# Optimization experiments

Measured on AMD Instinct MI355X. Metric: run time of the kernel, lower is better.

The kernel has to match this reference:

```python
import jax, jax.numpy as jnp
import numpy as np

DIM = 96
HEADS = 6
HEAD_DIM = DIM // HEADS
WIN = 8
N = WIN * WIN           # tokens per window
B_ = 4096               # num_windows * batch
TABLE = (2 * WIN - 1) ** 2  # 225


def setup_inputs() -> dict:
    key = jax.random.key(0)
    ks = jax.random.split(key, 7)
    x = jax.random.normal(ks[0], (B_, N, DIM), dtype=jnp.float32)
    rpi = jax.random.randint(ks[1], (N, N), 0, TABLE)
    qkv_w = jax.random.normal(ks[2], (3 * DIM, DIM), dtype=jnp.float32) * 0.02
    qkv_b = jnp.zeros((3 * DIM,), dtype=jnp.float32)
    proj_w = jax.random.normal(ks[3], (DIM, DIM), dtype=jnp.float32) * 0.02
    proj_b = jnp.zeros((DIM,), dtype=jnp.float32)
    rpb_table = jax.random.normal(ks[4], (TABLE, HEADS), dtype=jnp.float32) * 0.02
    return {"x": x, "rpi": rpi, "qkv_w": qkv_w, "qkv_b": qkv_b,
            "proj_w": proj_w, "proj_b": proj_b, "rpb_table": rpb_table}


def reference(x, rpi, qkv_w, qkv_b, proj_w, proj_b, rpb_table):
    b_, n, c = x.shape
    scale = HEAD_DIM ** -0.5
    # qkv projection: (b_, n, 3, H, hd)
    qkv = (x @ qkv_w.T + qkv_b).reshape(b_, n, 3, HEADS, HEAD_DIM)
    qkv = jnp.transpose(qkv, (2, 0, 3, 1, 4))  # (3, b_, H, n, hd)
    q, k, v = qkv[0], qkv[1], qkv[2]
    attn = jnp.einsum('bhnd,bhmd->bhnm', q * scale, k)
    # relative position bias gather: (n, n, H) -> (H, n, n)
    bias = jnp.transpose(rpb_table[rpi], (2, 0, 1))
    attn = jax.nn.softmax(attn + bias[None], axis=-1)
    out = jnp.einsum('bhnm,bhmd->bnhd', attn, v).reshape(b_, n, c)
    return out @ proj_w.T + proj_b
```

## Files before the change

kernel.cpp:

```cpp
#include <hip/hip_runtime.h>

#define NWIN 4096
#define DIM 96
#define HEADS 6
#define NTOK 64

typedef __bf16 bf16x8 __attribute__((ext_vector_type(8)));
typedef __bf16 bf16x4 __attribute__((ext_vector_type(4)));
typedef short  s16x4  __attribute__((ext_vector_type(4)));
typedef float  f32x4  __attribute__((ext_vector_type(4)));

#define WS_QKVW 0
#define WS_PROJW 55296
#define WS_BIAS 73728
#define WS_TOTAL 172032

__device__ __forceinline__ f32x4 mfma32(bf16x8 a, bf16x8 b, f32x4 c) {
  return __builtin_amdgcn_mfma_f32_16x16x32_bf16(a, b, c, 0, 0, 0);
}
__device__ __forceinline__ f32x4 mfma16k(bf16x4 a, bf16x4 b, f32x4 c) {
  return __builtin_amdgcn_mfma_f32_16x16x16bf16_1k(
      __builtin_bit_cast(s16x4, a), __builtin_bit_cast(s16x4, b), c, 0, 0, 0);
}

__device__ __forceinline__ bf16x8 cvt8(const float* p) {
  const float4* q = (const float4*)p;
  float4 a = q[0];
  float4 b = q[1];
  bf16x8 r;
  r[0] = (__bf16)a.x; r[1] = (__bf16)a.y; r[2] = (__bf16)a.z; r[3] = (__bf16)a.w;
  r[4] = (__bf16)b.x; r[5] = (__bf16)b.y; r[6] = (__bf16)b.z; r[7] = (__bf16)b.w;
  return r;
}

__global__ void prep_kernel(const float* __restrict__ qkv_w,
                            const float* __restrict__ proj_w,
                            const float* __restrict__ rpb,
                            const int* __restrict__ rpi,
                            char* __restrict__ ws) {
  int i = blockIdx.x * blockDim.x + threadIdx.x;
  __bf16* qw = (__bf16*)(ws + WS_QKVW);
  __bf16* pw = (__bf16*)(ws + WS_PROJW);
  float* bias = (float*)(ws + WS_BIAS);
  if (i < 288 * 96) qw[i] = (__bf16)qkv_w[i];
  int j = i - 288 * 96;
  if (j >= 0 && j < 96 * 96) pw[j] = (__bf16)proj_w[j];
  int t = i - (288 * 96 + 96 * 96);
  if (t >= 0 && t < HEADS * 16 * 64 * 4) {
    int r = t & 3;
    int lane = (t >> 2) & 63;
    int ba = (t >> 8) & 15;
    int h = t >> 12;
    int bq = ba >> 2, a = ba & 3;
    int l16 = lane & 15, lq = lane >> 4;
    int qrow = 16 * bq + l16;
    int kcol = 16 * a + 4 * lq + r;
    bias[t] = rpb[rpi[qrow * 64 + kcol] * HEADS + h];
  }
}

template <bool USE_WS>
__global__ __launch_bounds__(768, 4) void win_attn(
    const float* __restrict__ x,
    const int* __restrict__ rpi,
    const float* __restrict__ qkv_w,
    const float* __restrict__ qkv_b,
    const float* __restrict__ proj_w,
    const float* __restrict__ proj_b,
    const float* __restrict__ rpb,
    const char* __restrict__ ws,
    float* __restrict__ out) {
  __shared__ __align__(16) __bf16 lds[2 * 6656];

  const int tid = (int)threadIdx.x;
  const int wv = tid >> 6;
  const int win = wv / 6;
  const int h = wv - 6 * win;
  const int lane = tid & 63;
  const int l16 = lane & 15;
  const int lq = lane >> 4;
  const int b = 2 * (int)blockIdx.x + win;

  __bf16* xfrag = lds + win * 6656;
  __bf16* ao = xfrag;

  const float* xw = x + (size_t)b * (NTOK * DIM);
  const __bf16* qwb = (const __bf16*)(ws + WS_QKVW);
  const __bf16* pwb = (const __bf16*)(ws + WS_PROJW);
  const float4* bias4 = (const float4*)(ws + WS_BIAS) + (h << 10);

#pragma unroll
  for (int ff = 0; ff < 2; ++ff) {
    const int f = 2 * h + ff;
    const int mt = f / 3, ks = f - 3 * mt;
    bf16x8 v = cvt8(xw + (16 * mt + l16) * DIM + 32 * ks + 8 * lq);
    *(bf16x8*)(xfrag + (f * 64 + lane) * 8) = v;
  }
  __syncthreads();

#define XV(mt, ks) (*(const bf16x8*)(xfrag + (((mt) * 3 + (ks)) * 64 + lane) * 8))

  bf16x4 kb[4];
  {
    const int frow = (HEADS + h) * 16;
    bf16x8 wb[3];
#pragma unroll
    for (int ks = 0; ks < 3; ++ks) {
      if constexpr (USE_WS)
        wb[ks] = *(const bf16x8*)(qwb + (frow + l16) * 96 + 32 * ks + 8 * lq);
      else
        wb[ks] = cvt8(qkv_w + (frow + l16) * 96 + 32 * ks + 8 * lq);
    }
    const float4 kb4 = *(const float4*)(qkv_b + frow + 4 * lq);
    const float kbv[4] = {kb4.x, kb4.y, kb4.z, kb4.w};
#pragma unroll
    for (int mt = 0; mt < 4; ++mt) {
      f32x4 acc = {0.f, 0.f, 0.f, 0.f};
#pragma unroll
      for (int ks = 0; ks < 3; ++ks) acc = mfma32(wb[ks], XV(mt, ks), acc);
#pragma unroll
      for (int r = 0; r < 4; ++r) kb[mt][r] = (__bf16)(acc[r] + kbv[r]);
    }
  }

  bf16x4 qv4[4];
  {
    const int frow = h * 16;
    bf16x8 wb[3];
#pragma unroll
    for (int ks = 0; ks < 3; ++ks) {
      if constexpr (USE_WS)
        wb[ks] = *(const bf16x8*)(qwb + (frow + l16) * 96 + 32 * ks + 8 * lq);
      else
        wb[ks] = cvt8(qkv_w + (frow + l16) * 96 + 32 * ks + 8 * lq);
    }
    const float4 qb4 = *(const float4*)(qkv_b + frow + 4 * lq);
    const float qbv[4] = {qb4.x, qb4.y, qb4.z, qb4.w};
#pragma unroll
    for (int mt = 0; mt < 4; ++mt) {
      f32x4 acc = {0.f, 0.f, 0.f, 0.f};
#pragma unroll
      for (int ks = 0; ks < 3; ++ks) acc = mfma32(wb[ks], XV(mt, ks), acc);
#pragma unroll
      for (int r = 0; r < 4; ++r) qv4[mt][r] = (__bf16)((acc[r] + qbv[r]) * 0.25f);
    }
  }

  bf16x4 vb4[4];
  {
    const int frow = (2 * HEADS + h) * 16;
    bf16x8 wb[3];
#pragma unroll
    for (int ks = 0; ks < 3; ++ks) {
      if constexpr (USE_WS)
        wb[ks] = *(const bf16x8*)(qwb + (frow + l16) * 96 + 32 * ks + 8 * lq);
      else
        wb[ks] = cvt8(qkv_w + (frow + l16) * 96 + 32 * ks + 8 * lq);
    }
    const float vb = qkv_b[frow + l16];
#pragma unroll
    for (int mt = 0; mt < 4; ++mt) {
      f32x4 acc = {0.f, 0.f, 0.f, 0.f};
#pragma unroll
      for (int ks = 0; ks < 3; ++ks) acc = mfma32(XV(mt, ks), wb[ks], acc);
#pragma unroll
      for (int r = 0; r < 4; ++r) vb4[mt][r] = (__bf16)(acc[r] + vb);
    }
  }
#undef XV
  __syncthreads();

#pragma unroll
  for (int bq = 0; bq < 4; ++bq) {
    f32x4 s[4];
    if constexpr (USE_WS) {
#pragma unroll
      for (int a = 0; a < 4; ++a) {
        float4 t = bias4[(bq * 4 + a) * 64 + lane];
        s[a][0] = t.x; s[a][1] = t.y; s[a][2] = t.z; s[a][3] = t.w;
      }
    } else {
#pragma unroll
      for (int a = 0; a < 4; ++a)
#pragma unroll
        for (int r = 0; r < 4; ++r)
          s[a][r] = rpb[rpi[(16 * bq + l16) * 64 + 16 * a + 4 * lq + r] * HEADS + h];
    }

#pragma unroll
    for (int a = 0; a < 4; ++a) s[a] = mfma16k(kb[a], qv4[bq], s[a]);

    float tp[4];
    bf16x4 pa[4];
#pragma unroll
    for (int a = 0; a < 4; ++a) {
      float t0 = 0.f;
#pragma unroll
      for (int r = 0; r < 4; ++r) {
        const __bf16 pe = (__bf16)__expf(s[a][r]);
        pa[a][r] = pe;
        t0 += (float)pe;
      }
      tp[a] = t0;
    }
    float tsum = (tp[0] + tp[1]) + (tp[2] + tp[3]);
    tsum += __shfl_xor(tsum, 16);
    tsum += __shfl_xor(tsum, 32);

    f32x4 oacc = {0.f, 0.f, 0.f, 0.f};
#pragma unroll
    for (int a = 0; a < 4; ++a) oacc = mfma16k(pa[a], vb4[a], oacc);

    const float rv = 1.0f / tsum;
#pragma unroll
    for (int r = 0; r < 4; ++r)
      ao[(16 * bq + 4 * lq + r) * 104 + 16 * h + l16] = (__bf16)(oacc[r] * rv);
  }
  __syncthreads();

  bf16x8 wpb[3];
#pragma unroll
  for (int ks = 0; ks < 3; ++ks) {
    if constexpr (USE_WS)
      wpb[ks] = *(const bf16x8*)(pwb + (16 * h + l16) * 96 + 32 * ks + 8 * lq);
    else
      wpb[ks] = cvt8(proj_w + (16 * h + l16) * 96 + 32 * ks + 8 * lq);
  }
  const float pb2 = proj_b[16 * h + l16];
  float* outw = out + (size_t)b * (NTOK * DIM);
#pragma unroll
  for (int mt = 0; mt < 4; ++mt) {
    f32x4 acc = {0.f, 0.f, 0.f, 0.f};
#pragma unroll
    for (int ks = 0; ks < 3; ++ks) {
      bf16x8 aa = *(const bf16x8*)(ao + (16 * mt + l16) * 104 + 32 * ks + 8 * lq);
      acc = mfma32(aa, wpb[ks], acc);
    }
#pragma unroll
    for (int r = 0; r < 4; ++r)
      outw[(16 * mt + 4 * lq + r) * 96 + 16 * h + l16] = acc[r] + pb2;
  }
}

extern "C" void kernel_launch(void* const* d_in, const int* in_sizes, int n_in,
                              void* d_out, int out_size, void* d_ws, size_t ws_size,
                              hipStream_t stream) {
  const float* x      = (const float*)d_in[0];
  const int*   rpi    = (const int*)d_in[1];
  const float* qkv_w  = (const float*)d_in[2];
  const float* qkv_b  = (const float*)d_in[3];
  const float* proj_w = (const float*)d_in[4];
  const float* proj_b = (const float*)d_in[5];
  const float* rpb    = (const float*)d_in[6];
  float* out = (float*)d_out;

  if (ws_size >= (size_t)WS_TOTAL) {
    prep_kernel<<<240, 256, 0, stream>>>(qkv_w, proj_w, rpb, rpi, (char*)d_ws);
    win_attn<true><<<NWIN / 2, 768, 0, stream>>>(x, rpi, qkv_w, qkv_b, proj_w,
                                                 proj_b, rpb, (const char*)d_ws,
                                                 out);
  } else {
    win_attn<false><<<NWIN / 2, 768, 0, stream>>>(x, rpi, qkv_w, qkv_b, proj_w,
                                                  proj_b, rpb,
                                                  (const char*)d_ws, out);
  }
}
```

Before: 86.84 us.

## Use one window per 2-wave block, each wave looping over three heads

```diff
diff --git a/kernel.cpp b/kernel.cpp
--- a/kernel.cpp
+++ b/kernel.cpp
@@ -60,7 +60,7 @@
 }
 
 template <bool USE_WS>
-__global__ __launch_bounds__(768, 4) void win_attn(
+__global__ __launch_bounds__(128, 4) void win_attn(
     const float* __restrict__ x,
     const int* __restrict__ rpi,
     const float* __restrict__ qkv_w,
@@ -70,29 +70,25 @@
     const float* __restrict__ rpb,
     const char* __restrict__ ws,
     float* __restrict__ out) {
-  __shared__ __align__(16) __bf16 lds[2 * 6656];
+  __shared__ __align__(16) __bf16 xfrag[6144];
+  __shared__ __align__(16) __bf16 ao[64 * 104];
 
   const int tid = (int)threadIdx.x;
   const int wv = tid >> 6;
-  const int win = wv / 6;
-  const int h = wv - 6 * win;
   const int lane = tid & 63;
   const int l16 = lane & 15;
   const int lq = lane >> 4;
-  const int b = 2 * (int)blockIdx.x + win;
-
-  __bf16* xfrag = lds + win * 6656;
-  __bf16* ao = xfrag;
+  const int b = (int)blockIdx.x;
 
   const float* xw = x + (size_t)b * (NTOK * DIM);
   const __bf16* qwb = (const __bf16*)(ws + WS_QKVW);
   const __bf16* pwb = (const __bf16*)(ws + WS_PROJW);
-  const float4* bias4 = (const float4*)(ws + WS_BIAS) + (h << 10);
-
-#pragma unroll
-  for (int ff = 0; ff < 2; ++ff) {
-    const int f = 2 * h + ff;
-    const int mt = f / 3, ks = f - 3 * mt;
+
+#pragma unroll
+  for (int ff = 0; ff < 6; ++ff) {
+    const int mt = 2 * wv + ff / 3;
+    const int ks = ff % 3;
+    const int f = 6 * wv + ff;
     bf16x8 v = cvt8(xw + (16 * mt + l16) * DIM + 32 * ks + 8 * lq);
     *(bf16x8*)(xfrag + (f * 64 + lane) * 8) = v;
   }
@@ -100,145 +96,158 @@
 
 #define XV(mt, ks) (*(const bf16x8*)(xfrag + (((mt) * 3 + (ks)) * 64 + lane) * 8))
 
-  bf16x4 kb[4];
-  {
-    const int frow = (HEADS + h) * 16;
-    bf16x8 wb[3];
+#pragma unroll 1
+  for (int hh = 0; hh < 3; ++hh) {
+    const int h = wv + 2 * hh;
+
+    bf16x4 kb[4];
+    {
+      const int frow = (HEADS + h) * 16;
+      bf16x8 wb[3];
+#pragma unroll
+      for (int ks = 0; ks < 3; ++ks) {
+        if constexpr (USE_WS)
+          wb[ks] = *(const bf16x8*)(qwb + (frow + l16) * 96 + 32 * ks + 8 * lq);
+        else
+          wb[ks] = cvt8(qkv_w + (frow + l16) * 96 + 32 * ks + 8 * lq);
+      }
+      const float4 kb4 = *(const float4*)(qkv_b + frow + 4 * lq);
+      const float kbv[4] = {kb4.x, kb4.y, kb4.z, kb4.w};
+#pragma unroll
+      for (int mt = 0; mt < 4; ++mt) {
+        f32x4 acc = {0.f, 0.f, 0.f, 0.f};
+#pragma unroll
+        for (int ks = 0; ks < 3; ++ks) acc = mfma32(wb[ks], XV(mt, ks), acc);
+#pragma unroll
+        for (int r = 0; r < 4; ++r) kb[mt][r] = (__bf16)(acc[r] + kbv[r]);
+      }
+    }
+
+    bf16x4 qv4[4];
+    {
+      const int frow = h * 16;
+      bf16x8 wb[3];
+#pragma unroll
+      for (int ks = 0; ks < 3; ++ks) {
+        if constexpr (USE_WS)
+          wb[ks] = *(const bf16x8*)(qwb + (frow + l16) * 96 + 32 * ks + 8 * lq);
+        else
+          wb[ks] = cvt8(qkv_w + (frow + l16) * 96 + 32 * ks + 8 * lq);
+      }
+      const float4 qb4 = *(const float4*)(qkv_b + frow + 4 * lq);
+      const float qbv[4] = {qb4.x, qb4.y, qb4.z, qb4.w};
+#pragma unroll
+      for (int mt = 0; mt < 4; ++mt) {
+        f32x4 acc = {0.f, 0.f, 0.f, 0.f};
+#pragma unroll
+        for (int ks = 0; ks < 3; ++ks) acc = mfma32(wb[ks], XV(mt, ks), acc);
+#pragma unroll
+        for (int r = 0; r < 4; ++r)
+          qv4[mt][r] = (__bf16)((acc[r] + qbv[r]) * 0.25f);
+      }
+    }
+
+    bf16x4 vb4[4];
+    {
+      const int frow = (2 * HEADS + h) * 16;
+      bf16x8 wb[3];
+#pragma unroll
+      for (int ks = 0; ks < 3; ++ks) {
+        if constexpr (USE_WS)
+          wb[ks] = *(const bf16x8*)(qwb + (frow + l16) * 96 + 32 * ks + 8 * lq);
+        else
+          wb[ks] = cvt8(qkv_w + (frow + l16) * 96 + 32 * ks + 8 * lq);
+      }
+      const float vb = qkv_b[frow + l16];
+#pragma unroll
+      for (int mt = 0; mt < 4; ++mt) {
+        f32x4 acc = {0.f, 0.f, 0.f, 0.f};
+#pragma unroll
+        for (int ks = 0; ks < 3; ++ks) acc = mfma32(XV(mt, ks), wb[ks], acc);
+#pragma unroll
+        for (int r = 0; r < 4; ++r) vb4[mt][r] = (__bf16)(acc[r] + vb);
+      }
+    }
+
+    const float4* bias4 = (const float4*)(ws + WS_BIAS) + (h << 10);
+#pragma unroll
+    for (int bq = 0; bq < 4; ++bq) {
+      f32x4 s[4];
+      if constexpr (USE_WS) {
+#pragma unroll
+        for (int a = 0; a < 4; ++a) {
+          float4 t = bias4[(bq * 4 + a) * 64 + lane];
+          s[a][0] = t.x; s[a][1] = t.y; s[a][2] = t.z; s[a][3] = t.w;
+        }
+      } else {
+#pragma unroll
+        for (int a = 0; a < 4; ++a)
+#pragma unroll
+          for (int r = 0; r < 4; ++r)
+            s[a][r] = rpb[rpi[(16 * bq + l16) * 64 + 16 * a + 4 * lq + r] *
+                              HEADS + h];
+      }
+
+#pragma unroll
+      for (int a = 0; a < 4; ++a) s[a] = mfma16k(kb[a], qv4[bq], s[a]);
+
+      float tp[4];
+      bf16x4 pa[4];
+#pragma unroll
+      for (int a = 0; a < 4; ++a) {
+        float t0 = 0.f;
+#pragma unroll
+        for (int r = 0; r < 4; ++r) {
+          const __bf16 pe = (__bf16)__expf(s[a][r]);
+          pa[a][r] = pe;
+          t0 += (float)pe;
+        }
+        tp[a] = t0;
+      }
+      float tsum = (tp[0] + tp[1]) + (tp[2] + tp[3]);
+      tsum += __shfl_xor(tsum, 16);
+      tsum += __shfl_xor(tsum, 32);
+
+      f32x4 oacc = {0.f, 0.f, 0.f, 0.f};
+#pragma unroll
+      for (int a = 0; a < 4; ++a) oacc = mfma16k(pa[a], vb4[a], oacc);
+
+      const float rv = 1.0f / tsum;
+#pragma unroll
+      for (int r = 0; r < 4; ++r)
+        ao[(16 * bq + 4 * lq + r) * 104 + 16 * h + l16] =
+            (__bf16)(oacc[r] * rv);
+    }
+  }
+#undef XV
+  __syncthreads();
+
+  float* outw = out + (size_t)b * (NTOK * DIM);
+#pragma unroll 1
+  for (int cc = 0; cc < 3; ++cc) {
+    const int c = wv + 2 * cc;
+    bf16x8 wpb[3];
 #pragma unroll
     for (int ks = 0; ks < 3; ++ks) {
       if constexpr (USE_WS)
-        wb[ks] = *(const bf16x8*)(qwb + (frow + l16) * 96 + 32 * ks + 8 * lq);
+        wpb[ks] = *(const bf16x8*)(pwb + (16 * c + l16) * 96 + 32 * ks + 8 * lq);
       else
-        wb[ks] = cvt8(qkv_w + (frow + l16) * 96 + 32 * ks + 8 * lq);
-    }
-    const float4 kb4 = *(const float4*)(qkv_b + frow + 4 * lq);
-    const float kbv[4] = {kb4.x, kb4.y, kb4.z, kb4.w};
+        wpb[ks] = cvt8(proj_w + (16 * c + l16) * 96 + 32 * ks + 8 * lq);
+    }
+    const float pb2 = proj_b[16 * c + l16];
 #pragma unroll
     for (int mt = 0; mt < 4; ++mt) {
       f32x4 acc = {0.f, 0.f, 0.f, 0.f};
 #pragma unroll
-      for (int ks = 0; ks < 3; ++ks) acc = mfma32(wb[ks], XV(mt, ks), acc);
-#pragma unroll
-      for (int r = 0; r < 4; ++r) kb[mt][r] = (__bf16)(acc[r] + kbv[r]);
-    }
-  }
-
-  bf16x4 qv4[4];
-  {
-    const int frow = h * 16;
-    bf16x8 wb[3];
-#pragma unroll
-    for (int ks = 0; ks < 3; ++ks) {
-      if constexpr (USE_WS)
-        wb[ks] = *(const bf16x8*)(qwb + (frow + l16) * 96 + 32 * ks + 8 * lq);
-      else
-        wb[ks] = cvt8(qkv_w + (frow + l16) * 96 + 32 * ks + 8 * lq);
-    }
-    const float4 qb4 = *(const float4*)(qkv_b + frow + 4 * lq);
-    const float qbv[4] = {qb4.x, qb4.y, qb4.z, qb4.w};
-#pragma unroll
-    for (int mt = 0; mt < 4; ++mt) {
-      f32x4 acc = {0.f, 0.f, 0.f, 0.f};
-#pragma unroll
-      for (int ks = 0; ks < 3; ++ks) acc = mfma32(wb[ks], XV(mt, ks), acc);
-#pragma unroll
-      for (int r = 0; r < 4; ++r) qv4[mt][r] = (__bf16)((acc[r] + qbv[r]) * 0.25f);
-    }
-  }
-
-  bf16x4 vb4[4];
-  {
-    const int frow = (2 * HEADS + h) * 16;
-    bf16x8 wb[3];
-#pragma unroll
-    for (int ks = 0; ks < 3; ++ks) {
-      if constexpr (USE_WS)
-        wb[ks] = *(const bf16x8*)(qwb + (frow + l16) * 96 + 32 * ks + 8 * lq);
-      else
-        wb[ks] = cvt8(qkv_w + (frow + l16) * 96 + 32 * ks + 8 * lq);
-    }
-    const float vb = qkv_b[frow + l16];
-#pragma unroll
-    for (int mt = 0; mt < 4; ++mt) {
-      f32x4 acc = {0.f, 0.f, 0.f, 0.f};
-#pragma unroll
-      for (int ks = 0; ks < 3; ++ks) acc = mfma32(XV(mt, ks), wb[ks], acc);
-#pragma unroll
-      for (int r = 0; r < 4; ++r) vb4[mt][r] = (__bf16)(acc[r] + vb);
-    }
-  }
-#undef XV
-  __syncthreads();
-
-#pragma unroll
-  for (int bq = 0; bq < 4; ++bq) {
-    f32x4 s[4];
-    if constexpr (USE_WS) {
-#pragma unroll
-      for (int a = 0; a < 4; ++a) {
-        float4 t = bias4[(bq * 4 + a) * 64 + lane];
-        s[a][0] = t.x; s[a][1] = t.y; s[a][2] = t.z; s[a][3] = t.w;
-      }
-    } else {
-#pragma unroll
-      for (int a = 0; a < 4; ++a)
-#pragma unroll
-        for (int r = 0; r < 4; ++r)
-          s[a][r] = rpb[rpi[(16 * bq + l16) * 64 + 16 * a + 4 * lq + r] * HEADS + h];
-    }
-
-#pragma unroll
-    for (int a = 0; a < 4; ++a) s[a] = mfma16k(kb[a], qv4[bq], s[a]);
-
-    float tp[4];
-    bf16x4 pa[4];
-#pragma unroll
-    for (int a = 0; a < 4; ++a) {
-      float t0 = 0.f;
-#pragma unroll
-      for (int r = 0; r < 4; ++r) {
-        const __bf16 pe = (__bf16)__expf(s[a][r]);
-        pa[a][r] = pe;
-        t0 += (float)pe;
-      }
-      tp[a] = t0;
-    }
-    float tsum = (tp[0] + tp[1]) + (tp[2] + tp[3]);
-    tsum += __shfl_xor(tsum, 16);
-    tsum += __shfl_xor(tsum, 32);
-
-    f32x4 oacc = {0.f, 0.f, 0.f, 0.f};
-#pragma unroll
-    for (int a = 0; a < 4; ++a) oacc = mfma16k(pa[a], vb4[a], oacc);
-
-    const float rv = 1.0f / tsum;
-#pragma unroll
-    for (int r = 0; r < 4; ++r)
-      ao[(16 * bq + 4 * lq + r) * 104 + 16 * h + l16] = (__bf16)(oacc[r] * rv);
-  }
-  __syncthreads();
-
-  bf16x8 wpb[3];
-#pragma unroll
-  for (int ks = 0; ks < 3; ++ks) {
-    if constexpr (USE_WS)
-      wpb[ks] = *(const bf16x8*)(pwb + (16 * h + l16) * 96 + 32 * ks + 8 * lq);
-    else
-      wpb[ks] = cvt8(proj_w + (16 * h + l16) * 96 + 32 * ks + 8 * lq);
-  }
-  const float pb2 = proj_b[16 * h + l16];
-  float* outw = out + (size_t)b * (NTOK * DIM);
-#pragma unroll
-  for (int mt = 0; mt < 4; ++mt) {
-    f32x4 acc = {0.f, 0.f, 0.f, 0.f};
-#pragma unroll
-    for (int ks = 0; ks < 3; ++ks) {
-      bf16x8 aa = *(const bf16x8*)(ao + (16 * mt + l16) * 104 + 32 * ks + 8 * lq);
-      acc = mfma32(aa, wpb[ks], acc);
-    }
-#pragma unroll
-    for (int r = 0; r < 4; ++r)
-      outw[(16 * mt + 4 * lq + r) * 96 + 16 * h + l16] = acc[r] + pb2;
+      for (int ks = 0; ks < 3; ++ks) {
+        bf16x8 aa =
+            *(const bf16x8*)(ao + (16 * mt + l16) * 104 + 32 * ks + 8 * lq);
+        acc = mfma32(aa, wpb[ks], acc);
+      }
+#pragma unroll
+      for (int r = 0; r < 4; ++r)
+        outw[(16 * mt + 4 * lq + r) * 96 + 16 * c + l16] = acc[r] + pb2;
+    }
   }
 }
 
@@ -256,12 +265,12 @@
 
   if (ws_size >= (size_t)WS_TOTAL) {
     prep_kernel<<<240, 256, 0, stream>>>(qkv_w, proj_w, rpb, rpi, (char*)d_ws);
-    win_attn<true><<<NWIN / 2, 768, 0, stream>>>(x, rpi, qkv_w, qkv_b, proj_w,
-                                                 proj_b, rpb, (const char*)d_ws,
-                                                 out);
+    win_attn<true><<<NWIN, 128, 0, stream>>>(x, rpi, qkv_w, qkv_b, proj_w,
+                                             proj_b, rpb, (const char*)d_ws,
+                                             out);
   } else {
-    win_attn<false><<<NWIN / 2, 768, 0, stream>>>(x, rpi, qkv_w, qkv_b, proj_w,
-                                                  proj_b, rpb,
-                                                  (const char*)d_ws, out);
-  }
-}
+    win_attn<false><<<NWIN, 128, 0, stream>>>(x, rpi, qkv_w, qkv_b, proj_w,
+                                              proj_b, rpb, (const char*)d_ws,
+                                              out);
+  }
+}
```

Measured after the change: 81.55 us. -6.1%, faster.

## Process one window per single-wave block, looping heads and fusing projection

Applied to the files above, without the earlier changes.

```diff
diff --git a/kernel.cpp b/kernel.cpp
--- a/kernel.cpp
+++ b/kernel.cpp
@@ -9,11 +9,7 @@
 typedef __bf16 bf16x4 __attribute__((ext_vector_type(4)));
 typedef short  s16x4  __attribute__((ext_vector_type(4)));
 typedef float  f32x4  __attribute__((ext_vector_type(4)));
-
-#define WS_QKVW 0
-#define WS_PROJW 55296
-#define WS_BIAS 73728
-#define WS_TOTAL 172032
+typedef int    i32x4  __attribute__((ext_vector_type(4)));
 
 __device__ __forceinline__ f32x4 mfma32(bf16x8 a, bf16x8 b, f32x4 c) {
   return __builtin_amdgcn_mfma_f32_16x16x32_bf16(a, b, c, 0, 0, 0);
@@ -33,34 +29,14 @@
   return r;
 }
 
-__global__ void prep_kernel(const float* __restrict__ qkv_w,
-                            const float* __restrict__ proj_w,
-                            const float* __restrict__ rpb,
-                            const int* __restrict__ rpi,
-                            char* __restrict__ ws) {
-  int i = blockIdx.x * blockDim.x + threadIdx.x;
-  __bf16* qw = (__bf16*)(ws + WS_QKVW);
-  __bf16* pw = (__bf16*)(ws + WS_PROJW);
-  float* bias = (float*)(ws + WS_BIAS);
-  if (i < 288 * 96) qw[i] = (__bf16)qkv_w[i];
-  int j = i - 288 * 96;
-  if (j >= 0 && j < 96 * 96) pw[j] = (__bf16)proj_w[j];
-  int t = i - (288 * 96 + 96 * 96);
-  if (t >= 0 && t < HEADS * 16 * 64 * 4) {
-    int r = t & 3;
-    int lane = (t >> 2) & 63;
-    int ba = (t >> 8) & 15;
-    int h = t >> 12;
-    int bq = ba >> 2, a = ba & 3;
-    int l16 = lane & 15, lq = lane >> 4;
-    int qrow = 16 * bq + l16;
-    int kcol = 16 * a + 4 * lq + r;
-    bias[t] = rpb[rpi[qrow * 64 + kcol] * HEADS + h];
-  }
-}
-
-template <bool USE_WS>
-__global__ __launch_bounds__(768, 4) void win_attn(
+__device__ __forceinline__ bf16x4 cvt4(const float* p) {
+  const float4 t = *(const float4*)p;
+  bf16x4 r;
+  r[0] = (__bf16)t.x; r[1] = (__bf16)t.y; r[2] = (__bf16)t.z; r[3] = (__bf16)t.w;
+  return r;
+}
+
+__global__ __launch_bounds__(64, 2) void win_attn(
     const float* __restrict__ x,
     const int* __restrict__ rpi,
     const float* __restrict__ qkv_w,
@@ -68,31 +44,19 @@
     const float* __restrict__ proj_w,
     const float* __restrict__ proj_b,
     const float* __restrict__ rpb,
-    const char* __restrict__ ws,
     float* __restrict__ out) {
-  __shared__ __align__(16) __bf16 lds[2 * 6656];
-
-  const int tid = (int)threadIdx.x;
-  const int wv = tid >> 6;
-  const int win = wv / 6;
-  const int h = wv - 6 * win;
-  const int lane = tid & 63;
+  __shared__ __align__(16) __bf16 xfrag[6144];
+
+  const int lane = (int)threadIdx.x & 63;
   const int l16 = lane & 15;
   const int lq = lane >> 4;
-  const int b = 2 * (int)blockIdx.x + win;
-
-  __bf16* xfrag = lds + win * 6656;
-  __bf16* ao = xfrag;
+  const int b = (int)blockIdx.x;
 
   const float* xw = x + (size_t)b * (NTOK * DIM);
-  const __bf16* qwb = (const __bf16*)(ws + WS_QKVW);
-  const __bf16* pwb = (const __bf16*)(ws + WS_PROJW);
-  const float4* bias4 = (const float4*)(ws + WS_BIAS) + (h << 10);
-
-#pragma unroll
-  for (int ff = 0; ff < 2; ++ff) {
-    const int f = 2 * h + ff;
-    const int mt = f / 3, ks = f - 3 * mt;
+
+#pragma unroll
+  for (int f = 0; f < 12; ++f) {
+    const int mt = f / 3, ks = f % 3;
     bf16x8 v = cvt8(xw + (16 * mt + l16) * DIM + 32 * ks + 8 * lq);
     *(bf16x8*)(xfrag + (f * 64 + lane) * 8) = v;
   }
@@ -100,146 +64,133 @@
 
 #define XV(mt, ks) (*(const bf16x8*)(xfrag + (((mt) * 3 + (ks)) * 64 + lane) * 8))
 
-  bf16x4 kb[4];
-  {
-    const int frow = (HEADS + h) * 16;
-    bf16x8 wb[3];
-#pragma unroll
-    for (int ks = 0; ks < 3; ++ks) {
-      if constexpr (USE_WS)
-        wb[ks] = *(const bf16x8*)(qwb + (frow + l16) * 96 + 32 * ks + 8 * lq);
-      else
+  f32x4 pacc[4][6];
+#pragma unroll
+  for (int c = 0; c < 6; ++c) {
+    const float pb = proj_b[16 * c + l16];
+#pragma unroll
+    for (int bq = 0; bq < 4; ++bq) {
+      f32x4 t = {pb, pb, pb, pb};
+      pacc[bq][c] = t;
+    }
+  }
+
+#pragma unroll 1
+  for (int h = 0; h < HEADS; ++h) {
+    bf16x4 kb[4];
+    {
+      const int frow = (HEADS + h) * 16;
+      bf16x8 wb[3];
+#pragma unroll
+      for (int ks = 0; ks < 3; ++ks)
         wb[ks] = cvt8(qkv_w + (frow + l16) * 96 + 32 * ks + 8 * lq);
-    }
-    const float4 kb4 = *(const float4*)(qkv_b + frow + 4 * lq);
-    const float kbv[4] = {kb4.x, kb4.y, kb4.z, kb4.w};
-#pragma unroll
-    for (int mt = 0; mt < 4; ++mt) {
-      f32x4 acc = {0.f, 0.f, 0.f, 0.f};
-#pragma unroll
-      for (int ks = 0; ks < 3; ++ks) acc = mfma32(wb[ks], XV(mt, ks), acc);
-#pragma unroll
-      for (int r = 0; r < 4; ++r) kb[mt][r] = (__bf16)(acc[r] + kbv[r]);
-    }
-  }
-
-  bf16x4 qv4[4];
-  {
-    const int frow = h * 16;
-    bf16x8 wb[3];
-#pragma unroll
-    for (int ks = 0; ks < 3; ++ks) {
-      if constexpr (USE_WS)
-        wb[ks] = *(const bf16x8*)(qwb + (frow + l16) * 96 + 32 * ks + 8 * lq);
-      else
+      const float4 kb4 = *(const float4*)(qkv_b + frow + 4 * lq);
+#pragma unroll
+      for (int mt = 0; mt < 4; ++mt) {
+        f32x4 acc = {kb4.x, kb4.y, kb4.z, kb4.w};
+#pragma unroll
+        for (int ks = 0; ks < 3; ++ks) acc = mfma32(wb[ks], XV(mt, ks), acc);
+#pragma unroll
+        for (int r = 0; r < 4; ++r) kb[mt][r] = (__bf16)acc[r];
+      }
+    }
+
+    bf16x4 qv4[4];
+    {
+      const int frow = h * 16;
+      bf16x8 wb[3];
+#pragma unroll
+      for (int ks = 0; ks < 3; ++ks)
         wb[ks] = cvt8(qkv_w + (frow + l16) * 96 + 32 * ks + 8 * lq);
-    }
-    const float4 qb4 = *(const float4*)(qkv_b + frow + 4 * lq);
-    const float qbv[4] = {qb4.x, qb4.y, qb4.z, qb4.w};
-#pragma unroll
-    for (int mt = 0; mt < 4; ++mt) {
-      f32x4 acc = {0.f, 0.f, 0.f, 0.f};
-#pragma unroll
-      for (int ks = 0; ks < 3; ++ks) acc = mfma32(wb[ks], XV(mt, ks), acc);
-#pragma unroll
-      for (int r = 0; r < 4; ++r) qv4[mt][r] = (__bf16)((acc[r] + qbv[r]) * 0.25f);
-    }
-  }
-
-  bf16x4 vb4[4];
-  {
-    const int frow = (2 * HEADS + h) * 16;
-    bf16x8 wb[3];
-#pragma unroll
-    for (int ks = 0; ks < 3; ++ks) {
-      if constexpr (USE_WS)
-        wb[ks] = *(const bf16x8*)(qwb + (frow + l16) * 96 + 32 * ks + 8 * lq);
-      else
+      const float4 qb4 = *(const float4*)(qkv_b + frow + 4 * lq);
+#pragma unroll
+      for (int mt = 0; mt < 4; ++mt) {
+        f32x4 acc = {qb4.x, qb4.y, qb4.z, qb4.w};
+#pragma unroll
+        for (int ks = 0; ks < 3; ++ks) acc = mfma32(wb[ks], XV(mt, ks), acc);
+#pragma unroll
+        for (int r = 0; r < 4; ++r) qv4[mt][r] = (__bf16)(acc[r] * 0.25f);
+      }
+    }
+
+    bf16x4 vb4[4];
+    {
+      const int frow = (2 * HEADS + h) * 16;
+      bf16x8 wb[3];
+#pragma unroll
+      for (int ks = 0; ks < 3; ++ks)
         wb[ks] = cvt8(qkv_w + (frow + l16) * 96 + 32 * ks + 8 * lq);
-    }
-    const float vb = qkv_b[frow + l16];
-#pragma unroll
-    for (int mt = 0; mt < 4; ++mt) {
-      f32x4 acc = {0.f, 0.f, 0.f, 0.f};
-#pragma unroll
-      for (int ks = 0; ks < 3; ++ks) acc = mfma32(XV(mt, ks), wb[ks], acc);
-#pragma unroll
-      for (int r = 0; r < 4; ++r) vb4[mt][r] = (__bf16)(acc[r] + vb);
+      const float vb = qkv_b[frow + l16];
+#pragma unroll
+      for (int mt = 0; mt < 4; ++mt) {
+        f32x4 acc = {vb, vb, vb, vb};
+#pragma unroll
+        for (int ks = 0; ks < 3; ++ks) acc = mfma32(XV(mt, ks), wb[ks], acc);
+#pragma unroll
+        for (int r = 0; r < 4; ++r) vb4[mt][r] = (__bf16)acc[r];
+      }
+    }
+
+    bf16x4 wpch[6];
+#pragma unroll
+    for (int c = 0; c < 6; ++c)
+      wpch[c] = cvt4(proj_w + (16 * c + l16) * 96 + 16 * h + 4 * lq);
+
+#pragma unroll
+    for (int bq = 0; bq < 4; ++bq) {
+      f32x4 s[4];
+#pragma unroll
+      for (int a = 0; a < 4; ++a) {
+        const i32x4 idx =
+            *(const i32x4*)(rpi + (16 * bq + l16) * 64 + 16 * a + 4 * lq);
+#pragma unroll
+        for (int r = 0; r < 4; ++r) s[a][r] = rpb[idx[r] * HEADS + h];
+      }
+
+#pragma unroll
+      for (int a = 0; a < 4; ++a) s[a] = mfma16k(kb[a], qv4[bq], s[a]);
+
+      float tp[4];
+      bf16x4 pa[4];
+#pragma unroll
+      for (int a = 0; a < 4; ++a) {
+        float t0 = 0.f;
+#pragma unroll
+        for (int r = 0; r < 4; ++r) {
+          const __bf16 pe = (__bf16)__expf(s[a][r]);
+          pa[a][r] = pe;
+          t0 += (float)pe;
+        }
+        tp[a] = t0;
+      }
+      float tsum = (tp[0] + tp[1]) + (tp[2] + tp[3]);
+      tsum += __shfl_xor(tsum, 16);
+      tsum += __shfl_xor(tsum, 32);
+
+      f32x4 ot = {0.f, 0.f, 0.f, 0.f};
+#pragma unroll
+      for (int a = 0; a < 4; ++a) ot = mfma16k(vb4[a], pa[a], ot);
+
+      const float rv = 1.0f / tsum;
+      bf16x4 oat;
+#pragma unroll
+      for (int r = 0; r < 4; ++r) oat[r] = (__bf16)(ot[r] * rv);
+
+#pragma unroll
+      for (int c = 0; c < 6; ++c)
+        pacc[bq][c] = mfma16k(oat, wpch[c], pacc[bq][c]);
     }
   }
 #undef XV
-  __syncthreads();
-
-#pragma unroll
-  for (int bq = 0; bq < 4; ++bq) {
-    f32x4 s[4];
-    if constexpr (USE_WS) {
-#pragma unroll
-      for (int a = 0; a < 4; ++a) {
-        float4 t = bias4[(bq * 4 + a) * 64 + lane];
-        s[a][0] = t.x; s[a][1] = t.y; s[a][2] = t.z; s[a][3] = t.w;
-      }
-    } else {
-#pragma unroll
-      for (int a = 0; a < 4; ++a)
-#pragma unroll
-        for (int r = 0; r < 4; ++r)
-          s[a][r] = rpb[rpi[(16 * bq + l16) * 64 + 16 * a + 4 * lq + r] * HEADS + h];
-    }
-
-#pragma unroll
-    for (int a = 0; a < 4; ++a) s[a] = mfma16k(kb[a], qv4[bq], s[a]);
-
-    float tp[4];
-    bf16x4 pa[4];
-#pragma unroll
-    for (int a = 0; a < 4; ++a) {
-      float t0 = 0.f;
-#pragma unroll
-      for (int r = 0; r < 4; ++r) {
-        const __bf16 pe = (__bf16)__expf(s[a][r]);
-        pa[a][r] = pe;
-        t0 += (float)pe;
-      }
-      tp[a] = t0;
-    }
-    float tsum = (tp[0] + tp[1]) + (tp[2] + tp[3]);
-    tsum += __shfl_xor(tsum, 16);
-    tsum += __shfl_xor(tsum, 32);
-
-    f32x4 oacc = {0.f, 0.f, 0.f, 0.f};
-#pragma unroll
-    for (int a = 0; a < 4; ++a) oacc = mfma16k(pa[a], vb4[a], oacc);
-
-    const float rv = 1.0f / tsum;
-#pragma unroll
-    for (int r = 0; r < 4; ++r)
-      ao[(16 * bq + 4 * lq + r) * 104 + 16 * h + l16] = (__bf16)(oacc[r] * rv);
-  }
-  __syncthreads();
-
-  bf16x8 wpb[3];
-#pragma unroll
-  for (int ks = 0; ks < 3; ++ks) {
-    if constexpr (USE_WS)
-      wpb[ks] = *(const bf16x8*)(pwb + (16 * h + l16) * 96 + 32 * ks + 8 * lq);
-    else
-      wpb[ks] = cvt8(proj_w + (16 * h + l16) * 96 + 32 * ks + 8 * lq);
-  }
-  const float pb2 = proj_b[16 * h + l16];
+
   float* outw = out + (size_t)b * (NTOK * DIM);
 #pragma unroll
-  for (int mt = 0; mt < 4; ++mt) {
-    f32x4 acc = {0.f, 0.f, 0.f, 0.f};
-#pragma unroll
-    for (int ks = 0; ks < 3; ++ks) {
-      bf16x8 aa = *(const bf16x8*)(ao + (16 * mt + l16) * 104 + 32 * ks + 8 * lq);
-      acc = mfma32(aa, wpb[ks], acc);
-    }
-#pragma unroll
-    for (int r = 0; r < 4; ++r)
-      outw[(16 * mt + 4 * lq + r) * 96 + 16 * h + l16] = acc[r] + pb2;
-  }
+  for (int bq = 0; bq < 4; ++bq)
+#pragma unroll
+    for (int c = 0; c < 6; ++c)
+#pragma unroll
+      for (int r = 0; r < 4; ++r)
+        outw[(16 * bq + 4 * lq + r) * 96 + 16 * c + l16] = pacc[bq][c][r];
 }
 
 extern "C" void kernel_launch(void* const* d_in, const int* in_sizes, int n_in,
@@ -254,14 +205,6 @@
   const float* rpb    = (const float*)d_in[6];
   float* out = (float*)d_out;
 
-  if (ws_size >= (size_t)WS_TOTAL) {
-    prep_kernel<<<240, 256, 0, stream>>>(qkv_w, proj_w, rpb, rpi, (char*)d_ws);
-    win_attn<true><<<NWIN / 2, 768, 0, stream>>>(x, rpi, qkv_w, qkv_b, proj_w,
-                                                 proj_b, rpb, (const char*)d_ws,
-                                                 out);
-  } else {
-    win_attn<false><<<NWIN / 2, 768, 0, stream>>>(x, rpi, qkv_w, qkv_b, proj_w,
-                                                  proj_b, rpb,
-                                                  (const char*)d_ws, out);
-  }
-}
+  win_attn<<<NWIN, 64, 0, stream>>>(x, rpi, qkv_w, qkv_b, proj_w, proj_b,
+                                    rpb, out);
+}
```

Result: slower. 195.8 us (+125.5%).
